# Optimization experiments

Measured on AMD Instinct MI355X. Metric: run time of the kernel, lower is better.

The kernel has to match this reference:

```python
import jax, jax.numpy as jnp
import numpy as np

N, B, D, Q = 32, 36, 2048, 1024  # batch, objects, v_dim, q_dim


def setup_inputs() -> dict:
    key = jax.random.key(0)
    ks = jax.random.split(key, 6)
    sc = 0.02  # small init so ReLU chains stay well-scaled
    return {
        "v": jax.random.normal(ks[0], (N, B, D), jnp.float32),
        "q": jax.random.normal(ks[1], (N, Q), jnp.float32),
        "W1": jax.random.normal(ks[2], (D, D), jnp.float32) * sc,
        "b1": jnp.zeros((D,), jnp.float32),
        "W2": jax.random.normal(ks[3], (D, D), jnp.float32) * sc,
        "b2": jnp.zeros((D,), jnp.float32),
        "W3": jax.random.normal(ks[4], (Q, D), jnp.float32) * sc,
        "b3": jnp.zeros((D,), jnp.float32),
    }


def reference(v, q, W1, b1, W2, b2, W3, b3):
    # FCNet = ReLU(Linear(.)) with weight-norm folded, dropout=0 (eval).
    # Original calls linear3 twice (linear4 unused bug), so q_emb == q_emb2.
    qe = jax.nn.relu(q @ W3 + b3)  # (N, D)
    # pairs[n,i,j] = v[n,i]*qe[n] + v[n,j]*qe[n]  -> (N, B, B, D)
    pairs = (v[:, :, None, :] + v[:, None, :, :]) * qe[:, None, None, :]
    h = jax.nn.relu(jnp.einsum('nijd,de->nije', pairs, W1) + b1)  # linear1
    x = jnp.sum(h, axis=2)  # sum over j relations -> (N, B, D)
    return jax.nn.relu(x @ W2 + b2)  # linear2
```

## Files before the change

kernel.cpp:

```cpp
#include <hip/hip_runtime.h>
#include <stdint.h>

#define N_BATCH 32
#define B_OBJ   36
#define D_DIM   2048
#define Q_DIM   1024

typedef __bf16 bf16x8 __attribute__((ext_vector_type(8)));
typedef float  f32x4  __attribute__((ext_vector_type(4)));

__device__ __forceinline__ uint16_t f2bf(float f) {
    uint32_t u = __builtin_bit_cast(uint32_t, f);
    uint32_t r = (u + 0x7FFFu + ((u >> 16) & 1u)) >> 16;
    return (uint16_t)r;
}

__device__ __forceinline__ void gld_lds16(const void* g, void* l) {
    __builtin_amdgcn_global_load_lds(
        (const __attribute__((address_space(1))) uint32_t*)g,
        (__attribute__((address_space(3))) uint32_t*)l, 16, 0, 0);
}

__global__ __launch_bounds__(256) void transpose_all(
    const float* __restrict__ W1, const float* __restrict__ W2,
    const float* __restrict__ W3,
    uint16_t* __restrict__ W1t, uint16_t* __restrict__ W2t,
    uint16_t* __restrict__ W3t) {
    __shared__ float tile[64][65];
    int gy = blockIdx.y;
    const float* W; uint16_t* Wt; int K, k0;
    if (gy < 32)      { W = W1; Wt = W1t; K = 2048; k0 = gy * 64; }
    else if (gy < 64) { W = W2; Wt = W2t; K = 2048; k0 = (gy - 32) * 64; }
    else              { W = W3; Wt = W3t; K = 1024; k0 = (gy - 64) * 64; }
    int n0 = blockIdx.x * 64;
    int t = threadIdx.x;
    {
        int r = t >> 4, c = (t & 15) * 4;
#pragma unroll
        for (int p = 0; p < 4; ++p)
            *(float4*)&tile[r + p * 16][c] =
                *(const float4*)&W[(size_t)(k0 + r + p * 16) * 2048 + n0 + c];
    }
    __syncthreads();
    {
        int n = t >> 2, kb = (t & 3) * 16;
#pragma unroll
        for (int g4 = 0; g4 < 4; ++g4) {
            int k = kb + g4 * 4;
            ushort4 o;
            o.x = f2bf(tile[k][n]);     o.y = f2bf(tile[k + 1][n]);
            o.z = f2bf(tile[k + 2][n]); o.w = f2bf(tile[k + 3][n]);
            *(ushort4*)&Wt[(size_t)(n0 + n) * K + k0 + k] = o;
        }
    }
}

__global__ __launch_bounds__(256) void qk_gemm(
    const float* __restrict__ q,
    const uint16_t* __restrict__ W3t,
    float* __restrict__ qpart) {
    __shared__ __align__(16) uint16_t As[32][32];
    __shared__ __align__(16) uint16_t Bs[128][32];
    int t = threadIdx.x, lane = t & 63, wave = t >> 6;
    int l15 = lane & 15, quad = lane >> 4;
    int n0 = blockIdx.x * 128;
    int kbase = blockIdx.y * 256;
    f32x4 acc[2][2] = {};
    int ar = t >> 3, ac = (t & 7) * 4;
    int br = t >> 2, bk = (t & 3) * 8;

    for (int k0 = 0; k0 < 256; k0 += 32) {
        __syncthreads();
        float4 av = *(const float4*)&q[(size_t)ar * Q_DIM + kbase + k0 + ac];
        ushort4 a4;
        a4.x = f2bf(av.x); a4.y = f2bf(av.y); a4.z = f2bf(av.z); a4.w = f2bf(av.w);
        *(ushort4*)&As[ar][ac] = a4;
        *(uint4*)&Bs[br][bk]      = *(const uint4*)&W3t[(size_t)(n0 + br) * Q_DIM + kbase + k0 + bk];
        *(uint4*)&Bs[br + 64][bk] = *(const uint4*)&W3t[(size_t)(n0 + br + 64) * Q_DIM + kbase + k0 + bk];
        __syncthreads();
        bf16x8 af[2], bfr[2];
        af[0]  = *(const bf16x8*)&As[l15][quad * 8];
        af[1]  = *(const bf16x8*)&As[16 + l15][quad * 8];
        bfr[0] = *(const bf16x8*)&Bs[wave * 32 + l15][quad * 8];
        bfr[1] = *(const bf16x8*)&Bs[wave * 32 + 16 + l15][quad * 8];
#pragma unroll
        for (int i = 0; i < 2; ++i)
#pragma unroll
            for (int j = 0; j < 2; ++j)
                acc[i][j] = __builtin_amdgcn_mfma_f32_16x16x32_bf16(af[i], bfr[j], acc[i][j], 0, 0, 0);
    }
    float* dst = qpart + (size_t)blockIdx.y * 32 * D_DIM;
#pragma unroll
    for (int i = 0; i < 2; ++i)
#pragma unroll
        for (int j = 0; j < 2; ++j) {
            int n = n0 + wave * 32 + j * 16 + l15;
#pragma unroll
            for (int r = 0; r < 4; ++r)
                dst[(size_t)(i * 16 + quad * 4 + r) * D_DIM + n] = acc[i][j][r];
        }
}

__global__ __launch_bounds__(128) void qe_make_u(
    const float* __restrict__ qpart, const float* __restrict__ b3,
    const float* __restrict__ v, uint16_t* __restrict__ u) {
    int nb = blockIdx.y;
    int d4 = blockIdx.x * 128 + threadIdx.x;
    const float4* p = (const float4*)qpart;
    size_t base = (size_t)nb * 512 + d4;
    float4 s0 = p[base], s1 = p[16384 + base], s2 = p[32768 + base], s3 = p[49152 + base];
    float4 b = ((const float4*)b3)[d4];
    float4 qe;
    qe.x = fmaxf(s0.x + s1.x + s2.x + s3.x + b.x, 0.f);
    qe.y = fmaxf(s0.y + s1.y + s2.y + s3.y + b.y, 0.f);
    qe.z = fmaxf(s0.z + s1.z + s2.z + s3.z + b.z, 0.f);
    qe.w = fmaxf(s0.w + s1.w + s2.w + s3.w + b.w, 0.f);
    const float4* v4 = (const float4*)v;
    ushort4* u4 = (ushort4*)u;
    size_t rb = (size_t)nb * B_OBJ * 512 + d4;
#pragma unroll 4
    for (int i = 0; i < B_OBJ; ++i) {
        float4 vv = v4[rb + (size_t)i * 512];
        ushort4 o;
        o.x = f2bf(vv.x * qe.x);
        o.y = f2bf(vv.y * qe.y);
        o.z = f2bf(vv.z * qe.z);
        o.w = f2bf(vv.w * qe.w);
        u4[rb + (size_t)i * 512] = o;
    }
}

__global__ __launch_bounds__(256) void gemm_batch(
    const uint16_t* __restrict__ A,
    const uint16_t* __restrict__ Bt,
    const float* __restrict__ bias,
    void* __restrict__ Cv,
    int mode) {
    extern __shared__ __align__(16) uint16_t smem[];
    float* yt = (float*)smem;

    int t = threadIdx.x, lane = t & 63, wave = t >> 6;
    int l15 = lane & 15, quad = lane >> 4;
    int nb = blockIdx.y;
    int n0 = blockIdx.x * 128;
    const uint16_t* Ab = A + (size_t)nb * B_OBJ * D_DIM;

    const uint16_t* gp[6];
    int loff[6];
    int wslot = (lane & 3) ^ ((lane >> 2) & 3);
#pragma unroll
    for (int c = 0; c < 6; ++c) {
        int r = wave + 4 * c;
        int rr = (r < 22) ? r : 0;
        if (rr < 6) {
            int h = rr / 3, g = rr % 3;
            int row = g * 16 + (lane >> 2), kk = h * 32 + wslot * 8;
            gp[c] = Ab + (size_t)row * D_DIM + kk;
            loff[c] = h * 1536 + g * 512;
        } else {
            int rb = rr - 6, h = rb >> 3, g = rb & 7;
            int row = g * 16 + (lane >> 2), kk = h * 32 + wslot * 8;
            gp[c] = Bt + (size_t)(n0 + row) * D_DIM + kk;
            loff[c] = 3072 + h * 4096 + g * 512;
        }
    }

    f32x4 acc[3][2] = {};
    int rslot = quad ^ (l15 & 3);
    bool w01 = (wave < 2);

#define STAGE(kk, bi)                                                    \
    {                                                                    \
        _Pragma("unroll")                                                \
        for (int c = 0; c < 6; ++c)                                      \
            if (wave + 4 * c < 22)                                       \
                gld_lds16(gp[c] + (kk), smem + (bi) * 11264 + loff[c]);  \
    }

    STAGE(0, 0);
    STAGE(64, 1);
    STAGE(128, 2);
    if (w01) asm volatile("s_waitcnt vmcnt(12)" ::: "memory");
    else     asm volatile("s_waitcnt vmcnt(10)" ::: "memory");
    __builtin_amdgcn_s_barrier();

    int cur = 0;
    for (int k = 0; k < 32; ++k) {
        const uint16_t* As = smem + cur * 11264;
        const uint16_t* Bs = As + 3072;
#pragma unroll
        for (int s = 0; s < 2; ++s) {
            bf16x8 af[3], bfr[2];
#pragma unroll
            for (int i = 0; i < 3; ++i)
                af[i] = *(const bf16x8*)(As + s * 1536 + (i * 16 + l15) * 32 + rslot * 8);
#pragma unroll
            for (int j = 0; j < 2; ++j)
                bfr[j] = *(const bf16x8*)(Bs + s * 4096 + (wave * 32 + j * 16 + l15) * 32 + rslot * 8);
#pragma unroll
            for (int i = 0; i < 3; ++i)
#pragma unroll
                for (int j = 0; j < 2; ++j)
                    acc[i][j] = __builtin_amdgcn_mfma_f32_16x16x32_bf16(af[i], bfr[j], acc[i][j], 0, 0, 0);
        }
        if (k == 31) break;
        __builtin_amdgcn_s_barrier();
        if (k <= 28) {
            STAGE((k + 3) * 64, cur);
            if (w01) asm volatile("s_waitcnt vmcnt(12)" ::: "memory");
            else     asm volatile("s_waitcnt vmcnt(10)" ::: "memory");
        } else if (k == 29) {
            if (w01) asm volatile("s_waitcnt vmcnt(6)" ::: "memory");
            else     asm volatile("s_waitcnt vmcnt(5)" ::: "memory");
        } else {
            asm volatile("s_waitcnt vmcnt(0)" ::: "memory");
        }
        __builtin_amdgcn_s_barrier();
        cur = (cur == 2) ? 0 : cur + 1;
    }
#undef STAGE

    if (mode == 0) {
        uint16_t* X = (uint16_t*)Cv;
        __syncthreads();
#pragma unroll
        for (int i = 0; i < 3; ++i)
#pragma unroll
            for (int j = 0; j < 2; ++j)
#pragma unroll
                for (int r = 0; r < 4; ++r)
                    yt[(i * 16 + quad * 4 + r) * 132 + wave * 32 + j * 16 + l15] = acc[i][j][r];
        __syncthreads();
        int col = t & 127, half = t >> 7;
        float b = bias[n0 + col];
        float z[36];
#pragma unroll
        for (int j = 0; j < 36; ++j) z[j] = yt[j * 132 + col];
#pragma unroll
        for (int ii = 0; ii < 18; ++ii) {
            int i = half * 18 + ii;
            float zi = z[i] + b;
            float s = 0.f;
#pragma unroll
            for (int j = 0; j < 36; ++j) s += fmaxf(zi + z[j], 0.f);
            X[(size_t)(nb * B_OBJ + i) * D_DIM + n0 + col] = f2bf(s);
        }
    } else {
        float* O = (float*)Cv;
#pragma unroll
        for (int i = 0; i < 3; ++i)
#pragma unroll
            for (int r = 0; r < 4; ++r) {
                int row = i * 16 + quad * 4 + r;
                if (row < B_OBJ) {
#pragma unroll
                    for (int j = 0; j < 2; ++j) {
                        int cc = n0 + wave * 32 + j * 16 + l15;
                        O[(size_t)(nb * B_OBJ + row) * D_DIM + cc] =
                            fmaxf(acc[i][j][r] + bias[cc], 0.f);
                    }
                }
            }
    }
}

extern "C" void kernel_launch(void* const* d_in, const int* in_sizes, int n_in,
                              void* d_out, int out_size, void* d_ws, size_t ws_size,
                              hipStream_t stream) {
    const float* v  = (const float*)d_in[0];
    const float* q  = (const float*)d_in[1];
    const float* W1 = (const float*)d_in[2];
    const float* b1 = (const float*)d_in[3];
    const float* W2 = (const float*)d_in[4];
    const float* b2 = (const float*)d_in[5];
    const float* W3 = (const float*)d_in[6];
    const float* b3 = (const float*)d_in[7];
    float* out = (float*)d_out;

    char* ws = (char*)d_ws;
    uint16_t* W1t   = (uint16_t*)(ws + 0);
    uint16_t* W2t   = (uint16_t*)(ws + 8388608);
    uint16_t* W3t   = (uint16_t*)(ws + 16777216);
    uint16_t* u     = (uint16_t*)(ws + 16777216);
    float*    qpart = (float*)   (ws + 21495808);
    uint16_t* x     = (uint16_t*)(ws + 22806528);

    static bool attr_done = false;
    if (!attr_done) {
        (void)hipFuncSetAttribute((const void*)gemm_batch,
                                  hipFuncAttributeMaxDynamicSharedMemorySize, 67584);
        attr_done = true;
    }

    transpose_all<<<dim3(32, 80), 256, 0, stream>>>(W1, W2, W3, W1t, W2t, W3t);

    qk_gemm<<<dim3(16, 4), 256, 0, stream>>>(q, W3t, qpart);

    qe_make_u<<<dim3(4, N_BATCH), 128, 0, stream>>>(qpart, b3, v, u);

    gemm_batch<<<dim3(16, N_BATCH), 256, 67584, stream>>>(u, W1t, b1, x, 0);

    gemm_batch<<<dim3(16, N_BATCH), 256, 67584, stream>>>(x, W2t, b2, out, 1);
}
```

Before: 176.3 us.

## Process two batch items per 512-thread block to share W tile loads

The batched GEMM block now handles two batch elements (96 padded rows) with 8 waves in a 2x4 layout, so each loaded W1/W2 column tile is reused across both batches. Pipelining drops from triple to double buffering in static shared memory (about 57KB), and the grid halves to 256 blocks. The aim is to cut global/L2 traffic for the weight matrices. In exchange there are fewer blocks than CUs' worth of parallelism and a shallower prefetch depth, which could expose load latency.

```diff
diff --git a/kernel.cpp b/kernel.cpp
--- a/kernel.cpp
+++ b/kernel.cpp
@@ -130,73 +130,76 @@
     }
 }
 
-__global__ __launch_bounds__(256) void gemm_batch(
+__global__ __launch_bounds__(512) void gemm_batch(
     const uint16_t* __restrict__ A,
     const uint16_t* __restrict__ Bt,
     const float* __restrict__ bias,
     void* __restrict__ Cv,
     int mode) {
-    extern __shared__ __align__(16) uint16_t smem[];
-    float* yt = (float*)smem;
+    __shared__ __align__(16) uint16_t smem[2][14336];
+    float* yt = (float*)&smem[0][0];
 
     int t = threadIdx.x, lane = t & 63, wave = t >> 6;
     int l15 = lane & 15, quad = lane >> 4;
-    int nb = blockIdx.y;
+    int wr = wave >> 2, wc = wave & 3;
+    int nbp = blockIdx.y;
     int n0 = blockIdx.x * 128;
-    const uint16_t* Ab = A + (size_t)nb * B_OBJ * D_DIM;
-
-    const uint16_t* gp[6];
-    int loff[6];
+    const uint16_t* Ab = A + (size_t)nbp * 72 * D_DIM;
+
+    const uint16_t* gp[4];
+    int loff[4];
     int wslot = (lane & 3) ^ ((lane >> 2) & 3);
 #pragma unroll
-    for (int c = 0; c < 6; ++c) {
-        int r = wave + 4 * c;
-        int rr = (r < 22) ? r : 0;
-        if (rr < 6) {
-            int h = rr / 3, g = rr % 3;
-            int row = g * 16 + (lane >> 2), kk = h * 32 + wslot * 8;
-            gp[c] = Ab + (size_t)row * D_DIM + kk;
-            loff[c] = h * 1536 + g * 512;
+    for (int c = 0; c < 4; ++c) {
+        int r = wave + 8 * c;
+        int rr = (r < 28) ? r : 0;
+        if (rr < 12) {
+            int g = rr >> 1, h = rr & 1;
+            int arow = g * 16 + (lane >> 2) - (g >= 3 ? 12 : 0);
+            gp[c] = Ab + (size_t)arow * D_DIM + h * 32 + wslot * 8;
+            loff[c] = h * 3072 + g * 512;
         } else {
-            int rb = rr - 6, h = rb >> 3, g = rb & 7;
-            int row = g * 16 + (lane >> 2), kk = h * 32 + wslot * 8;
-            gp[c] = Bt + (size_t)(n0 + row) * D_DIM + kk;
-            loff[c] = 3072 + h * 4096 + g * 512;
+            int rb = rr - 12, g = rb >> 1, h = rb & 1;
+            int brow = g * 16 + (lane >> 2);
+            gp[c] = Bt + (size_t)(n0 + brow) * D_DIM + h * 32 + wslot * 8;
+            loff[c] = 6144 + h * 4096 + g * 512;
         }
     }
 
     f32x4 acc[3][2] = {};
     int rslot = quad ^ (l15 & 3);
-    bool w01 = (wave < 2);
-
-#define STAGE(kk, bi)                                                    \
-    {                                                                    \
-        _Pragma("unroll")                                                \
-        for (int c = 0; c < 6; ++c)                                      \
-            if (wave + 4 * c < 22)                                       \
-                gld_lds16(gp[c] + (kk), smem + (bi) * 11264 + loff[c]);  \
+
+#define STAGE(kk, bi)                                    \
+    {                                                    \
+        _Pragma("unroll")                                \
+        for (int c = 0; c < 4; ++c)                      \
+            if (wave + 8 * c < 28)                       \
+                gld_lds16(gp[c] + (kk), &smem[bi][loff[c]]); \
+    }
+#define WAIT_L()                                                      \
+    {                                                                 \
+        if (wave < 4) asm volatile("s_waitcnt vmcnt(4)" ::: "memory");\
+        else          asm volatile("s_waitcnt vmcnt(3)" ::: "memory");\
     }
 
     STAGE(0, 0);
     STAGE(64, 1);
-    STAGE(128, 2);
-    if (w01) asm volatile("s_waitcnt vmcnt(12)" ::: "memory");
-    else     asm volatile("s_waitcnt vmcnt(10)" ::: "memory");
+    WAIT_L();
     __builtin_amdgcn_s_barrier();
 
-    int cur = 0;
     for (int k = 0; k < 32; ++k) {
-        const uint16_t* As = smem + cur * 11264;
-        const uint16_t* Bs = As + 3072;
+        int cur = k & 1;
+        const uint16_t* As = &smem[cur][0];
+        const uint16_t* Bs = As + 6144;
 #pragma unroll
         for (int s = 0; s < 2; ++s) {
             bf16x8 af[3], bfr[2];
 #pragma unroll
             for (int i = 0; i < 3; ++i)
-                af[i] = *(const bf16x8*)(As + s * 1536 + (i * 16 + l15) * 32 + rslot * 8);
+                af[i] = *(const bf16x8*)(As + s * 3072 + (wr * 48 + i * 16 + l15) * 32 + rslot * 8);
 #pragma unroll
             for (int j = 0; j < 2; ++j)
-                bfr[j] = *(const bf16x8*)(Bs + s * 4096 + (wave * 32 + j * 16 + l15) * 32 + rslot * 8);
+                bfr[j] = *(const bf16x8*)(Bs + s * 4096 + (wc * 32 + j * 16 + l15) * 32 + rslot * 8);
 #pragma unroll
             for (int i = 0; i < 3; ++i)
 #pragma unroll
@@ -205,20 +208,16 @@
         }
         if (k == 31) break;
         __builtin_amdgcn_s_barrier();
-        if (k <= 28) {
-            STAGE((k + 3) * 64, cur);
-            if (w01) asm volatile("s_waitcnt vmcnt(12)" ::: "memory");
-            else     asm volatile("s_waitcnt vmcnt(10)" ::: "memory");
-        } else if (k == 29) {
-            if (w01) asm volatile("s_waitcnt vmcnt(6)" ::: "memory");
-            else     asm volatile("s_waitcnt vmcnt(5)" ::: "memory");
+        if (k < 30) {
+            STAGE((k + 2) * 64, cur);
+            WAIT_L();
         } else {
             asm volatile("s_waitcnt vmcnt(0)" ::: "memory");
         }
         __builtin_amdgcn_s_barrier();
-        cur = (cur == 2) ? 0 : cur + 1;
     }
 #undef STAGE
+#undef WAIT_L
 
     if (mode == 0) {
         uint16_t* X = (uint16_t*)Cv;
@@ -229,21 +228,22 @@
             for (int j = 0; j < 2; ++j)
 #pragma unroll
                 for (int r = 0; r < 4; ++r)
-                    yt[(i * 16 + quad * 4 + r) * 132 + wave * 32 + j * 16 + l15] = acc[i][j][r];
-        __syncthreads();
-        int col = t & 127, half = t >> 7;
-        float b = bias[n0 + col];
+                    yt[(wr * 48 + i * 16 + quad * 4 + r) * 132 + wc * 32 + j * 16 + l15] = acc[i][j][r];
+        __syncthreads();
+        int col = t & 127, sub = t >> 7;
+        int b = sub >> 1, half = sub & 1;
+        float bv = bias[n0 + col];
         float z[36];
 #pragma unroll
-        for (int j = 0; j < 36; ++j) z[j] = yt[j * 132 + col];
+        for (int j = 0; j < 36; ++j) z[j] = yt[(b * 48 + j) * 132 + col];
 #pragma unroll
         for (int ii = 0; ii < 18; ++ii) {
             int i = half * 18 + ii;
-            float zi = z[i] + b;
+            float zi = z[i] + bv;
             float s = 0.f;
 #pragma unroll
             for (int j = 0; j < 36; ++j) s += fmaxf(zi + z[j], 0.f);
-            X[(size_t)(nb * B_OBJ + i) * D_DIM + n0 + col] = f2bf(s);
+            X[(size_t)((nbp * 2 + b) * B_OBJ + i) * D_DIM + n0 + col] = f2bf(s);
         }
     } else {
         float* O = (float*)Cv;
@@ -251,12 +251,12 @@
         for (int i = 0; i < 3; ++i)
 #pragma unroll
             for (int r = 0; r < 4; ++r) {
-                int row = i * 16 + quad * 4 + r;
-                if (row < B_OBJ) {
+                int obj = i * 16 + quad * 4 + r;
+                if (obj < B_OBJ) {
 #pragma unroll
                     for (int j = 0; j < 2; ++j) {
-                        int cc = n0 + wave * 32 + j * 16 + l15;
-                        O[(size_t)(nb * B_OBJ + row) * D_DIM + cc] =
+                        int cc = n0 + wc * 32 + j * 16 + l15;
+                        O[(size_t)((nbp * 2 + wr) * B_OBJ + obj) * D_DIM + cc] =
                             fmaxf(acc[i][j][r] + bias[cc], 0.f);
                     }
                 }
@@ -285,20 +285,13 @@
     float*    qpart = (float*)   (ws + 21495808);
     uint16_t* x     = (uint16_t*)(ws + 22806528);
 
-    static bool attr_done = false;
-    if (!attr_done) {
-        (void)hipFuncSetAttribute((const void*)gemm_batch,
-                                  hipFuncAttributeMaxDynamicSharedMemorySize, 67584);
-        attr_done = true;
-    }
-
     transpose_all<<<dim3(32, 80), 256, 0, stream>>>(W1, W2, W3, W1t, W2t, W3t);
 
     qk_gemm<<<dim3(16, 4), 256, 0, stream>>>(q, W3t, qpart);
 
     qe_make_u<<<dim3(4, N_BATCH), 128, 0, stream>>>(qpart, b3, v, u);
 
-    gemm_batch<<<dim3(16, N_BATCH), 256, 67584, stream>>>(u, W1t, b1, x, 0);
-
-    gemm_batch<<<dim3(16, N_BATCH), 256, 67584, stream>>>(x, W2t, b2, out, 1);
-}
+    gemm_batch<<<dim3(16, 16), 512, 0, stream>>>(u, W1t, b1, x, 0);
+
+    gemm_batch<<<dim3(16, 16), 512, 0, stream>>>(x, W2t, b2, out, 1);
+}
```

Result: faster. 171.9 us (-2.5%).
